# Optimization experiments

Measured on AMD Instinct MI355X. Metric: run time of the kernel, lower is better.

## Reference

```python
import jax, jax.numpy as jnp
import numpy as np

N, E = 10000, 160000          # nodes, support edges
CIN, COUT = 32, 32            # channels
R, B = 6, 1                   # radial rings, band limit
M = 2 * B + 1                 # angular frequencies (-B..B)
EPS = 1e-8
PI = float(np.pi)


def _cplx(a):
    # (..., 2) real -> complex64
    return jax.lax.complex(a[..., 0], a[..., 1])


def _reim(z):
    # complex -> (..., 2) real
    return jnp.stack([jnp.real(z), jnp.imag(z)], axis=-1)


def _field_conv(xc, edges, stenc, w, off):
    """FieldConv (ftype=1): real radial/angular weights with per-channel phase offsets.
    xc: (N,Cin) complex, stenc: (E,R,M) complex stencil (transport+quadrature pre-multiplied),
    w: (R,M,Cin,Cout) real, off: (Cin,Cout) phase offsets."""
    Wc = w * jax.lax.complex(jnp.cos(off), jnp.sin(off))[None, None]   # (R,M,Cin,Cout) complex
    src, tgt = edges[:, 0], edges[:, 1]
    # edge gather + complex stencil multiply: (E,R,M,Cin)
    contrib = stenc[:, :, :, None] * xc[src][:, None, None, :]
    # scatter-add to target nodes: (N,R,M,Cin)
    agg = jax.ops.segment_sum(contrib, tgt, num_segments=N)
    # dense per-node filter contraction
    return jnp.einsum('nrmc,rmcd->nd', agg, Wc)


def _tangent_nonlin(xc, b):
    # magnitude ReLU with learned bias, direction preserved (complex tangent features)
    mag = jnp.abs(xc)
    return (jax.nn.relu(mag + b) / jnp.maximum(mag, EPS)) * xc


def _forward(x, supp_edges, supp_sten, w1, off1, b1, w2, off2, b2, res_w):
    xc = _cplx(x)                # (N,CIN) complex64
    stenc = _cplx(supp_sten)     # (E,R,M) complex64
    h = _tangent_nonlin(_field_conv(xc, supp_edges, stenc, w1, off1), b1)
    h = _field_conv(h, supp_edges, stenc, w2, off2)
    y = _tangent_nonlin(xc @ _cplx(res_w) + h, b2)   # residual TangentLin + nonlin
    return _reim(y)              # (N,COUT,2) float32


def setup_inputs() -> dict:
    key = jax.random.key(0)
    ks = jax.random.split(key, 10)
    s1 = 1.0 / np.sqrt(R * M * CIN)
    s2 = 1.0 / np.sqrt(R * M * COUT)
    return {
        'x': jax.random.normal(ks[0], (N, CIN, 2), jnp.float32),
        'supp_edges': jax.random.randint(ks[1], (E, 2), 0, N),
        'supp_sten': 0.1 * jax.random.normal(ks[2], (E, R, M, 2), jnp.float32),
        'w1': s1 * jax.random.normal(ks[3], (R, M, CIN, COUT), jnp.float32),
        'off1': jax.random.uniform(ks[4], (CIN, COUT), jnp.float32, -PI, PI),
        'b1': 0.1 * jax.random.normal(ks[5], (COUT,), jnp.float32),
        'w2': s2 * jax.random.normal(ks[6], (R, M, COUT, COUT), jnp.float32),
        'off2': jax.random.uniform(ks[7], (COUT, COUT), jnp.float32, -PI, PI),
        'b2': 0.1 * jax.random.normal(ks[8], (COUT,), jnp.float32),
        'res_w': (1.0 / np.sqrt(CIN)) * jax.random.normal(ks[9], (CIN, COUT, 2), jnp.float32),
    }


def reference(x, supp_edges, supp_sten, w1, off1, b1, w2, off2, b2, res_w):
    return _forward(x, supp_edges, supp_sten, w1, off1, b1, w2, off2, b2, res_w)
```

## Files before the change

### kernel.cpp

```cpp
#include <hip/hip_runtime.h>

#define NN   10000
#define EE   160000
#define CINC 32
#define COUTC 32
#define RRR  6
#define MMM  3
#define RM   (RRR*MMM)
#define KK   (RM*CINC)
#define NPB  4
#define CAP  64
#define AROW 592
#define WSZ  18432
#define EPSV 1e-8f

typedef __attribute__((ext_vector_type(8))) short bf16x8;
typedef __attribute__((ext_vector_type(4))) float f32x4;
typedef __attribute__((ext_vector_type(16))) float f32x16;

__device__ inline short f2bf(float f) {
    unsigned u = __float_as_uint(f);
    u = (u + 0x7FFF + ((u >> 16) & 1)) >> 16;
    return (short)u;
}
__device__ inline float bf2f(unsigned short h) {
    return __uint_as_float(((unsigned)h) << 16);
}
__device__ inline uint2 packsplit(float re, float im) {
    unsigned short rh = (unsigned short)f2bf(re);
    unsigned short rl = (unsigned short)f2bf(re - bf2f(rh));
    unsigned short ih = (unsigned short)f2bf(im);
    unsigned short il = (unsigned short)f2bf(im - bf2f(ih));
    return make_uint2((unsigned)rh | ((unsigned)rl << 16),
                      (unsigned)ih | ((unsigned)il << 16));
}

__global__ void __launch_bounds__(256)
k_build(const int* __restrict__ edges, int* __restrict__ cursor,
        const float* __restrict__ w1, const float* __restrict__ off1,
        const float* __restrict__ w2, const float* __restrict__ off2,
        short* __restrict__ Wcb1, short* __restrict__ Wcb2,
        int2* __restrict__ sei,
        const float2* __restrict__ xc, uint2* __restrict__ xbf)
{
    int i = blockIdx.x*blockDim.x + threadIdx.x;
    if (i < KK*COUTC) {
        int d = i & 31;
        int k = i >> 5;
        int c = k & 31;
        int r_ = k >> 5;
        int q  = (k >> 3) & 3;
        int kk = k & 7;
        int l  = q*16 + (d & 15);
        int n2 = d >> 4;
        int addr = ((r_*2 + n2)*64 + l)*8 + kk;
        float o1 = off1[c*COUTC + d];
        float o2 = off2[c*COUTC + d];
        float s1 = sinf(o1), c1 = cosf(o1);
        float s2 = sinf(o2), c2 = cosf(o2);
        Wcb1[addr]       = f2bf(w1[i]*c1);
        Wcb1[WSZ + addr] = f2bf(w1[i]*s1);
        Wcb2[addr]       = f2bf(w2[i]*c2);
        Wcb2[WSZ + addr] = f2bf(w2[i]*s2);
    }
    if (i < EE) {
        int src = edges[2*i];
        int tgt = edges[2*i+1];
        int pos = atomicAdd(&cursor[tgt], 1);
        if (pos < CAP) sei[tgt*CAP + pos] = make_int2(src, i);
    }
    if (i < NN*CINC) {
        float2 v = xc[i];
        xbf[i] = packsplit(v.x, v.y);
    }
}

__global__ void __launch_bounds__(1024)
k_order(const int* __restrict__ cnts, int* __restrict__ order) {
    __shared__ int bins[CAP+1];
    __shared__ int suf[128];
    __shared__ int base[CAP+1];
    int t = threadIdx.x;
    if (t <= CAP) bins[t] = 0;
    __syncthreads();
    for (int n = t; n < NN; n += 1024) {
        int d = cnts[n]; if (d > CAP) d = CAP;
        atomicAdd(&bins[d], 1);
    }
    __syncthreads();
    if (t < 128) suf[t] = (t <= CAP) ? bins[t] : 0;
    __syncthreads();
    #pragma unroll
    for (int s = 1; s < 128; s <<= 1) {
        int v = 0;
        if (t < 128 && t + s < 128) v = suf[t+s];
        __syncthreads();
        if (t < 128) suf[t] += v;
        __syncthreads();
    }
    if (t <= CAP) base[t] = (t+1 < 128) ? suf[t+1] : 0;
    __syncthreads();
    for (int n = t; n < NN; n += 1024) {
        int d = cnts[n]; if (d > CAP) d = CAP;
        int r = atomicAdd(&base[d], 1);
        order[r] = n;
    }
}


template<bool FINAL>
__global__ void __launch_bounds__(256)
k_conv(const uint2* __restrict__ xbf,
       const int*  __restrict__ cnts,
       const int*  __restrict__ order,
       const int2* __restrict__ sei,
       const float4* __restrict__ stenc4,
       const short* __restrict__ Wcb,
       const float* __restrict__ bias,
       const float2* __restrict__ xres,
       const float2* __restrict__ resw,
       float2* __restrict__ out,
       uint2* __restrict__ outbf)
{
    __shared__ __align__(16) short aggS[2*NPB*AROW];
    __shared__ int nid[NPB];
    int t = threadIdx.x;
    int g = t >> 6;
    int l = t & 63;
    int c = l & 31;
    int oct = l >> 5;

    f32x16 Pre = (f32x16)(0.f), Pim = (f32x16)(0.f);
    {
        int n = order[blockIdx.x*NPB + g];
        if (l == 0) nid[g] = n;
        int cnt = cnts[n]; if (cnt > CAP) cnt = CAP;
        int srcAll = 0, eidAll = 0;
        if (l < cnt) { int2 v = sei[n*CAP + l]; srcAll = v.x; eidAll = v.y; }

        bool rmok = (c < RM);
        int rmo = ((c >> 1) << 4) + ((c & 1) << 3);
        const char* sb = (const char*)stenc4;
        int ntiles = (cnt + 15) >> 4;

        union P { unsigned u[4]; short s[8]; bf16x8 v; };

        for (int ck = 0; ck < ntiles; ++ck) {
            int ebase = ck*16 + oct*8;
            float2 sv[8];
            uint2  xv[8];
            #pragma unroll
            for (int j = 0; j < 8; ++j) {
                int e = ebase + j;
                int eid = __shfl(eidAll, e, 64);
                int s   = __shfl(srcAll, e, 64);
                bool ok = rmok && (e < cnt);
                float2 vv = make_float2(0.f, 0.f);
                if (ok) vv = *(const float2*)(sb + (size_t)eid*144 + rmo);
                sv[j] = vv;
                xv[j] = xbf[(s << 5) | c];
            }
            P Are, Aim, AimN;
            #pragma unroll
            for (int j = 0; j < 8; ++j) {
                Are.s[j] = f2bf(sv[j].x);
                Aim.s[j] = f2bf(sv[j].y);
            }
            #pragma unroll
            for (int k2 = 0; k2 < 4; ++k2) AimN.u[k2] = Aim.u[k2] ^ 0x80008000u;

            P B;
            #pragma unroll
            for (int k2 = 0; k2 < 4; ++k2)
                B.u[k2] = (xv[2*k2].x & 0xffffu) | (xv[2*k2+1].x << 16);
            Pre = __builtin_amdgcn_mfma_f32_32x32x16_bf16(Are.v, B.v, Pre, 0, 0, 0);
            Pim = __builtin_amdgcn_mfma_f32_32x32x16_bf16(Aim.v, B.v, Pim, 0, 0, 0);
            #pragma unroll
            for (int k2 = 0; k2 < 4; ++k2)
                B.u[k2] = (xv[2*k2].x >> 16) | (xv[2*k2+1].x & 0xffff0000u);
            Pre = __builtin_amdgcn_mfma_f32_32x32x16_bf16(Are.v, B.v, Pre, 0, 0, 0);
            Pim = __builtin_amdgcn_mfma_f32_32x32x16_bf16(Aim.v, B.v, Pim, 0, 0, 0);
            #pragma unroll
            for (int k2 = 0; k2 < 4; ++k2)
                B.u[k2] = (xv[2*k2].y & 0xffffu) | (xv[2*k2+1].y << 16);
            Pre = __builtin_amdgcn_mfma_f32_32x32x16_bf16(AimN.v, B.v, Pre, 0, 0, 0);
            Pim = __builtin_amdgcn_mfma_f32_32x32x16_bf16(Are.v, B.v, Pim, 0, 0, 0);
            #pragma unroll
            for (int k2 = 0; k2 < 4; ++k2)
                B.u[k2] = (xv[2*k2].y >> 16) | (xv[2*k2+1].y & 0xffff0000u);
            Pre = __builtin_amdgcn_mfma_f32_32x32x16_bf16(AimN.v, B.v, Pre, 0, 0, 0);
            Pim = __builtin_amdgcn_mfma_f32_32x32x16_bf16(Are.v, B.v, Pim, 0, 0, 0);
        }

        short* aR = aggS + g*AROW;
        short* aI = aggS + NPB*AROW + g*AROW;
        #pragma unroll
        for (int reg = 0; reg < 16; ++reg) {
            int rm = (reg & 3) + 8*(reg >> 2) + 4*oct;
            if (rm < RM) {
                aR[rm*32 + c] = f2bf(Pre[reg]);
                aI[rm*32 + c] = f2bf(Pim[reg]);
            }
        }
    }
    __syncthreads();

    int quad = l >> 4;
    int nn16 = l & 15;
    int mrow = (nn16 < NPB) ? nn16 : NPB-1;
    int rm0 = (g < 2) ? 5*g : 10 + 4*(g-2);
    int nrm = (g < 2) ? 5 : 4;
    const short* aggR = aggS;
    const short* aggI = aggS + NPB*AROW;
    const short* Wr = Wcb;
    const short* Wi = Wcb + WSZ;
    int lbase = l*8;

    f32x4 Prr[2], Pii[2], Pri[2], Pir[2];
    #pragma unroll
    for (int nt = 0; nt < 2; ++nt) {
        Prr[nt] = (f32x4)(0.f); Pii[nt] = (f32x4)(0.f);
        Pri[nt] = (f32x4)(0.f); Pir[nt] = (f32x4)(0.f);
    }
    for (int r = rm0; r < rm0 + nrm; ++r) {
        int koff = r*32 + quad*8;
        bf16x8 ar = *(const bf16x8*)(aggR + mrow*AROW + koff);
        bf16x8 ai = *(const bf16x8*)(aggI + mrow*AROW + koff);
        #pragma unroll
        for (int nt = 0; nt < 2; ++nt) {
            int woff = ((r*2 + nt) << 9) + lbase;
            bf16x8 br = *(const bf16x8*)(Wr + woff);
            bf16x8 bi = *(const bf16x8*)(Wi + woff);
            Prr[nt] = __builtin_amdgcn_mfma_f32_16x16x32_bf16(ar, br, Prr[nt], 0, 0, 0);
            Pii[nt] = __builtin_amdgcn_mfma_f32_16x16x32_bf16(ai, bi, Pii[nt], 0, 0, 0);
            Pri[nt] = __builtin_amdgcn_mfma_f32_16x16x32_bf16(ar, bi, Pri[nt], 0, 0, 0);
            Pir[nt] = __builtin_amdgcn_mfma_f32_16x16x32_bf16(ai, br, Pir[nt], 0, 0, 0);
        }
    }
    __syncthreads();

    float2* dump = (float2*)aggS;
    if (quad == 0) {
        #pragma unroll
        for (int reg = 0; reg < 4; ++reg) {
            int m = reg;
            #pragma unroll
            for (int nt = 0; nt < 2; ++nt) {
                int d = nt*16 + nn16;
                dump[((size_t)g*NPB + m)*COUTC + d] =
                    make_float2(Prr[nt][reg] - Pii[nt][reg],
                                Pri[nt][reg] + Pir[nt][reg]);
            }
        }
    }
    __syncthreads();

    if (t < NPB*COUTC) {
        int m = t >> 5, d = t & 31;
        int n = nid[m];
        float2 hv = make_float2(0.f, 0.f);
        #pragma unroll
        for (int w = 0; w < NPB; ++w) {
            float2 v = dump[((size_t)w*NPB + m)*COUTC + d];
            hv.x += v.x; hv.y += v.y;
        }
        if (FINAL) {
            const float2* xr = xres + (size_t)n * CINC;
            #pragma unroll
            for (int cc = 0; cc < CINC; ++cc) {
                float2 xv = xr[cc];
                float2 w = resw[cc*COUTC + d];
                hv.x += xv.x*w.x - xv.y*w.y;
                hv.y += xv.x*w.y + xv.y*w.x;
            }
        }
        float mag = sqrtf(hv.x*hv.x + hv.y*hv.y);
        float num = mag + bias[d]; if (num < 0.f) num = 0.f;
        float den = (mag > EPSV) ? mag : EPSV;
        float f = num / den;
        if (FINAL) out[(size_t)n*COUTC + d] = make_float2(f*hv.x, f*hv.y);
        else       outbf[(size_t)n*COUTC + d] = packsplit(f*hv.x, f*hv.y);
    }
}


extern "C" void kernel_launch(void* const* d_in, const int* in_sizes, int n_in,
                              void* d_out, int out_size, void* d_ws, size_t ws_size,
                              hipStream_t stream) {
    const float2* xc   = (const float2*)d_in[0];
    const int*   edges = (const int*)  d_in[1];
    const float4* stenc4 = (const float4*)d_in[2];
    const float* w1    = (const float*)d_in[3];
    const float* off1  = (const float*)d_in[4];
    const float* b1    = (const float*)d_in[5];
    const float* w2    = (const float*)d_in[6];
    const float* off2  = (const float*)d_in[7];
    const float* b2    = (const float*)d_in[8];
    const float2* resw = (const float2*)d_in[9];
    float2* out = (float2*)d_out;

    char* ws = (char*)d_ws;
    size_t o = 0;
    auto alloc = [&](size_t bytes) {
        o = (o + 255) & ~(size_t)255;
        size_t r = o; o += bytes; return r;
    };
    int*    cursor = (int*)  (ws + alloc(NN*sizeof(int)));
    int*    order  = (int*)  (ws + alloc(NN*sizeof(int)));
    int2*   sei    = (int2*) (ws + alloc((size_t)NN*CAP*sizeof(int2)));
    short*  Wcb1   = (short*)(ws + alloc((size_t)2*WSZ*sizeof(short)));
    short*  Wcb2   = (short*)(ws + alloc((size_t)2*WSZ*sizeof(short)));
    uint2*  xbf    = (uint2*)(ws + alloc((size_t)NN*CINC*sizeof(uint2)));
    uint2*  hbf    = (uint2*)(ws + alloc((size_t)NN*CINC*sizeof(uint2)));
    (void)ws_size; (void)in_sizes; (void)n_in; (void)out_size;

    hipMemsetAsync(cursor, 0, NN*sizeof(int), stream);
    k_build<<<(NN*CINC + 255)/256, 256, 0, stream>>>(edges, cursor, w1, off1, w2, off2,
                                                     Wcb1, Wcb2, sei, xc, xbf);
    k_order<<<1, 1024, 0, stream>>>(cursor, order);

    k_conv<false><<<NN/NPB, 256, 0, stream>>>(xbf, cursor, order, sei, stenc4,
                                              Wcb1, b1, nullptr, nullptr, nullptr, hbf);
    k_conv<true> <<<NN/NPB, 256, 0, stream>>>(hbf, cursor, order, sei, stenc4,
                                              Wcb2, b2, xc, resw, out, nullptr);
}
```

Baseline: 156.2 us.

## Fold residual TangentLin into MFMA filter contraction as extra K block

Appends the residual linear weights as a 19th K-block of the packed bf16 filter matrix, with the node's input features written into the shared aggregate row. The scalar 32-step complex residual loop in the epilogue is then no longer needed. The degree count is also packed together with the node id in the order array, so one uncoalesced cursor load per node is skipped, and bf16 conversion now uses the library intrinsic. This removes serial per-thread FMA work and a gather at the cost of slightly more LDS and one more MFMA K-block. Residual precision drops from fp32 to single bf16 on both the inputs and the weights.

```diff
diff --git a/kernel.cpp b/kernel.cpp
--- a/kernel.cpp
+++ b/kernel.cpp
@@ -1,4 +1,5 @@
 #include <hip/hip_runtime.h>
+#include <hip/hip_bf16.h>
 
 #define NN   10000
 #define EE   160000
@@ -8,10 +9,11 @@
 #define MMM  3
 #define RM   (RRR*MMM)
 #define KK   (RM*CINC)
+#define KE   608
 #define NPB  4
 #define CAP  64
-#define AROW 592
-#define WSZ  18432
+#define AROW 624
+#define WSZ  19456
 #define EPSV 1e-8f
 
 typedef __attribute__((ext_vector_type(8))) short bf16x8;
@@ -19,9 +21,9 @@
 typedef __attribute__((ext_vector_type(16))) float f32x16;
 
 __device__ inline short f2bf(float f) {
-    unsigned u = __float_as_uint(f);
-    u = (u + 0x7FFF + ((u >> 16) & 1)) >> 16;
-    return (short)u;
+    __hip_bfloat16 b = __float2bfloat16(f);
+    union { __hip_bfloat16 b; short s; } u; u.b = b;
+    return u.s;
 }
 __device__ inline float bf2f(unsigned short h) {
     return __uint_as_float(((unsigned)h) << 16);
@@ -41,7 +43,8 @@
         const float* __restrict__ w2, const float* __restrict__ off2,
         short* __restrict__ Wcb1, short* __restrict__ Wcb2,
         int2* __restrict__ sei,
-        const float2* __restrict__ xc, uint2* __restrict__ xbf)
+        const float2* __restrict__ xc, uint2* __restrict__ xbf,
+        const float2* __restrict__ resw)
 {
     int i = blockIdx.x*blockDim.x + threadIdx.x;
     if (i < KK*COUTC) {
@@ -63,6 +66,19 @@
         Wcb2[addr]       = f2bf(w2[i]*c2);
         Wcb2[WSZ + addr] = f2bf(w2[i]*s2);
     }
+    if (i < 1024) {
+        int n2 = i >> 9;
+        int l2 = (i >> 3) & 63;
+        int kk = i & 7;
+        int c  = ((l2 >> 4) << 3) + kk;
+        int d  = (n2 << 4) + (l2 & 15);
+        int addr = ((18*2 + n2)*64 + l2)*8 + kk;
+        float2 rv = resw[c*COUTC + d];
+        Wcb2[addr]       = f2bf(rv.x);
+        Wcb2[WSZ + addr] = f2bf(rv.y);
+        Wcb1[addr]       = 0;
+        Wcb1[WSZ + addr] = 0;
+    }
     if (i < EE) {
         int src = edges[2*i];
         int tgt = edges[2*i+1];
@@ -76,7 +92,7 @@
 }
 
 __global__ void __launch_bounds__(1024)
-k_order(const int* __restrict__ cnts, int* __restrict__ order) {
+k_order(const int* __restrict__ cnts, int2* __restrict__ order2) {
     __shared__ int bins[CAP+1];
     __shared__ int suf[128];
     __shared__ int base[CAP+1];
@@ -103,22 +119,19 @@
     for (int n = t; n < NN; n += 1024) {
         int d = cnts[n]; if (d > CAP) d = CAP;
         int r = atomicAdd(&base[d], 1);
-        order[r] = n;
-    }
-}
-
+        order2[r] = make_int2(n, d);
+    }
+}
 
 template<bool FINAL>
 __global__ void __launch_bounds__(256)
 k_conv(const uint2* __restrict__ xbf,
-       const int*  __restrict__ cnts,
-       const int*  __restrict__ order,
+       const int2* __restrict__ order2,
        const int2* __restrict__ sei,
        const float4* __restrict__ stenc4,
        const short* __restrict__ Wcb,
        const float* __restrict__ bias,
        const float2* __restrict__ xres,
-       const float2* __restrict__ resw,
        float2* __restrict__ out,
        uint2* __restrict__ outbf)
 {
@@ -131,10 +144,12 @@
     int oct = l >> 5;
 
     f32x16 Pre = (f32x16)(0.f), Pim = (f32x16)(0.f);
+    int n;
     {
-        int n = order[blockIdx.x*NPB + g];
+        int2 hdr = order2[blockIdx.x*NPB + g];
+        n = hdr.x;
+        int cnt = hdr.y;
         if (l == 0) nid[g] = n;
-        int cnt = cnts[n]; if (cnt > CAP) cnt = CAP;
         int srcAll = 0, eidAll = 0;
         if (l < cnt) { int2 v = sei[n*CAP + l]; srcAll = v.x; eidAll = v.y; }
 
@@ -202,14 +217,20 @@
                 aI[rm*32 + c] = f2bf(Pim[reg]);
             }
         }
+        if (l < 32) {
+            float2 xv = make_float2(0.f, 0.f);
+            if (FINAL) xv = xres[(size_t)n*CINC + l];
+            aR[KK + l] = f2bf(xv.x);
+            aI[KK + l] = f2bf(xv.y);
+        }
     }
     __syncthreads();
 
     int quad = l >> 4;
     int nn16 = l & 15;
     int mrow = (nn16 < NPB) ? nn16 : NPB-1;
-    int rm0 = (g < 2) ? 5*g : 10 + 4*(g-2);
-    int nrm = (g < 2) ? 5 : 4;
+    int rm0 = (g < 3) ? 5*g : 15;
+    int nrm = (g < 3) ? 5 : 4;
     const short* aggR = aggS;
     const short* aggI = aggS + NPB*AROW;
     const short* Wr = Wcb;
@@ -257,32 +278,21 @@
 
     if (t < NPB*COUTC) {
         int m = t >> 5, d = t & 31;
-        int n = nid[m];
+        int nn = nid[m];
         float2 hv = make_float2(0.f, 0.f);
         #pragma unroll
         for (int w = 0; w < NPB; ++w) {
             float2 v = dump[((size_t)w*NPB + m)*COUTC + d];
             hv.x += v.x; hv.y += v.y;
         }
-        if (FINAL) {
-            const float2* xr = xres + (size_t)n * CINC;
-            #pragma unroll
-            for (int cc = 0; cc < CINC; ++cc) {
-                float2 xv = xr[cc];
-                float2 w = resw[cc*COUTC + d];
-                hv.x += xv.x*w.x - xv.y*w.y;
-                hv.y += xv.x*w.y + xv.y*w.x;
-            }
-        }
         float mag = sqrtf(hv.x*hv.x + hv.y*hv.y);
         float num = mag + bias[d]; if (num < 0.f) num = 0.f;
         float den = (mag > EPSV) ? mag : EPSV;
         float f = num / den;
-        if (FINAL) out[(size_t)n*COUTC + d] = make_float2(f*hv.x, f*hv.y);
-        else       outbf[(size_t)n*COUTC + d] = packsplit(f*hv.x, f*hv.y);
-    }
-}
-
+        if (FINAL) out[(size_t)nn*COUTC + d] = make_float2(f*hv.x, f*hv.y);
+        else       outbf[(size_t)nn*COUTC + d] = packsplit(f*hv.x, f*hv.y);
+    }
+}
 
 extern "C" void kernel_launch(void* const* d_in, const int* in_sizes, int n_in,
                               void* d_out, int out_size, void* d_ws, size_t ws_size,
@@ -306,7 +316,7 @@
         size_t r = o; o += bytes; return r;
     };
     int*    cursor = (int*)  (ws + alloc(NN*sizeof(int)));
-    int*    order  = (int*)  (ws + alloc(NN*sizeof(int)));
+    int2*   order2 = (int2*) (ws + alloc(NN*sizeof(int2)));
     int2*   sei    = (int2*) (ws + alloc((size_t)NN*CAP*sizeof(int2)));
     short*  Wcb1   = (short*)(ws + alloc((size_t)2*WSZ*sizeof(short)));
     short*  Wcb2   = (short*)(ws + alloc((size_t)2*WSZ*sizeof(short)));
@@ -316,11 +326,11 @@
 
     hipMemsetAsync(cursor, 0, NN*sizeof(int), stream);
     k_build<<<(NN*CINC + 255)/256, 256, 0, stream>>>(edges, cursor, w1, off1, w2, off2,
-                                                     Wcb1, Wcb2, sei, xc, xbf);
-    k_order<<<1, 1024, 0, stream>>>(cursor, order);
-
-    k_conv<false><<<NN/NPB, 256, 0, stream>>>(xbf, cursor, order, sei, stenc4,
-                                              Wcb1, b1, nullptr, nullptr, nullptr, hbf);
-    k_conv<true> <<<NN/NPB, 256, 0, stream>>>(hbf, cursor, order, sei, stenc4,
-                                              Wcb2, b2, xc, resw, out, nullptr);
-}
+                                                     Wcb1, Wcb2, sei, xc, xbf, resw);
+    k_order<<<1, 1024, 0, stream>>>(cursor, order2);
+
+    k_conv<false><<<NN/NPB, 256, 0, stream>>>(xbf, order2, sei, stenc4,
+                                              Wcb1, b1, nullptr, nullptr, hbf);
+    k_conv<true> <<<NN/NPB, 256, 0, stream>>>(hbf, order2, sei, stenc4,
+                                              Wcb2, b2, xc, out, nullptr);
+}
```

Measured after the change: 149.3 us. 1.05x faster.
